# Kernel tuning notes

Hardware: AMD Instinct MI355X
Metric: run time of the kernel (lower is better)

## Reference

```python
import jax, jax.numpy as jnp
import numpy as np

N, E, B = 20000, 320000, 2
IN, HID, HEADS, OUT = 32, 64, 4, 8
N_MP = 2
SLOPE = 0.2  # GATConv default negative_slope


def setup_inputs() -> dict:
    key = jax.random.key(0)
    ks = jax.random.split(key, 10)
    s = 0.1
    return {
        "h": jax.random.normal(ks[0], (B, N, IN), jnp.float32),
        "edge_index": jax.random.randint(ks[1], (2, E), 0, N),
        "W_enc": jax.random.normal(ks[2], (IN, HID), jnp.float32) * s,
        "b_enc": jnp.zeros((HID,), jnp.float32),
        "W_gat": jax.random.normal(ks[3], (HID, HEADS * HID), jnp.float32) * s,
        "a_l": jax.random.normal(ks[4], (HEADS, HID), jnp.float32) * s,
        "a_r": jax.random.normal(ks[5], (HEADS, HID), jnp.float32) * s,
        "b_gat": jnp.zeros((HEADS * HID,), jnp.float32),
        "W_res": jax.random.normal(ks[6], (HID, HID), jnp.float32) * s,
        "b_res": jnp.zeros((HID,), jnp.float32),
        "W_dec": jax.random.normal(ks[7], (HID, OUT), jnp.float32) * s,
        "b_dec": jnp.zeros((OUT,), jnp.float32),
    }


def _gat(x, src, dst, W_gat, a_l, a_r, b_gat):
    # x: [N, B, HID] -> per-head projected features [N, B, HEADS, HID]
    ft = (x @ W_gat).reshape(N, B, HEADS, HID)
    el = jnp.einsum("nbhd,hd->nbh", ft, a_l)  # src attention term
    er = jnp.einsum("nbhd,hd->nbh", ft, a_r)  # dst attention term
    e = el[src] + er[dst]                      # [E, B, HEADS]
    e = jnp.where(e > 0, e, SLOPE * e)         # LeakyReLU
    # segment softmax over incoming edges of each dst node
    m = jax.ops.segment_max(e, dst, num_segments=N)
    e = jnp.exp(e - m[dst])
    z = jax.ops.segment_sum(e, dst, num_segments=N)
    alpha = e / z[dst]                         # [E, B, HEADS]
    msg = alpha[..., None] * ft[src]           # [E, B, HEADS, HID]
    agg = jax.ops.segment_sum(msg, dst, num_segments=N)
    return agg + b_gat.reshape(HEADS, HID)     # [N, B, HEADS, HID]


def reference(h, edge_index, W_enc, b_enc, W_gat, a_l, a_r, b_gat,
              W_res, b_res, W_dec, b_dec):
    src, dst = edge_index[0], edge_index[1]
    x = jnp.transpose(h, (1, 0, 2))            # [N, B, IN]
    x = x @ W_enc + b_enc                      # encoder (dropout in eval = identity)
    for _ in range(N_MP):
        gat_out = _gat(x, src, dst, W_gat, a_l, a_r, b_gat)
        x = jax.nn.elu(gat_out.mean(-2) + x @ W_res + b_res)
    x = x @ W_dec + b_dec
    return jnp.transpose(x, (1, 0, 2))         # [B, N, OUT]
```

## Files before the change

kernel.cpp:

```cpp
#include <hip/hip_runtime.h>
#include <hip/hip_bf16.h>

#define N_NODES 20000
#define N_EDGES 320000
#define BATCH 2
#define IN_DIM 32
#define HID 64
#define HEADS 4
#define OUT_DIM 8
#define ROWS (N_NODES * BATCH)
#define SLOPE 0.2f

typedef __hip_bfloat16 bf16;
typedef short v8s __attribute__((ext_vector_type(8)));
typedef float v4f __attribute__((ext_vector_type(4)));

#define WS_XA       0
#define WS_XB       1280000
#define WS_ELA      2560000
#define WS_ERA      2720000
#define WS_ELB      2880000
#define WS_ERB      3040000
#define WS_DEG      3200000
#define WS_ROWSTART 3220032
#define WS_CUR      3240064
#define WS_CSRC     3260096
#define WS_WGBPK    3580096
#define WS_WRESBPK  3588288
#define WS_WX8PK    3590336
#define WS_WENCBPK  3590848
#define WS_WDECBPK  3591872
#define WS_BGM      3592384
#define WS_END      3592448

__device__ __forceinline__ float us2f(unsigned short u) {
    union { unsigned int i; float f; } z; z.i = ((unsigned int)u) << 16; return z.f;
}
__device__ __forceinline__ unsigned short f2us(float f) {
    bf16 b = __float2bfloat16(f);
    return *(unsigned short*)&b;
}
__device__ __forceinline__ float ld(const void* p, int i, int isbf) {
    if (isbf) return us2f(((const unsigned short*)p)[i]);
    return ((const float*)p)[i];
}
__device__ __forceinline__ float lrexp(float v) {
    v = v > 0.f ? v : SLOPE * v;
    return __expf(fminf(v, 60.f));
}

__device__ __forceinline__ int sniff64(const void* h) {
    const unsigned short* u = (const unsigned short*)h;
    int lane = threadIdx.x & 63;
    unsigned short v = u[2 * lane];
    int ef = (v >> 7) & 0xFF;
    unsigned long long m = __ballot(ef >= 100 && ef <= 150);
    return __popcll(m) >= 48;
}

__global__ __launch_bounds__(256) void k_prep(const void* __restrict__ h,
                                              const void* __restrict__ Wg,
                                              const void* __restrict__ al,
                                              const void* __restrict__ ar,
                                              const void* __restrict__ Wr,
                                              const void* __restrict__ We,
                                              const void* __restrict__ Wd,
                                              const void* __restrict__ bg,
                                              unsigned short* __restrict__ WgBpk,
                                              unsigned short* __restrict__ WresBpk,
                                              unsigned short* __restrict__ Wx8pk,
                                              unsigned short* __restrict__ WencBpk,
                                              unsigned short* __restrict__ WdecBpk,
                                              float* __restrict__ bgm,
                                              int* __restrict__ deg) {
    int t = threadIdx.x, b = blockIdx.x;
    if (b >= 18) {
        int base = (b - 18) * 1024 + t * 4;
#pragma unroll
        for (int i = 0; i < 4; i++)
            if (base + i < 20032) deg[base + i] = 0;
        return;
    }
    const int isbf = sniff64(h);
    if (b < 16) {
#pragma unroll
        for (int q = 0; q < 4; q++) {
            int idx = b * 1024 + q * 256 + t;
            int j = idx & 7, m16 = (idx >> 3) & 15, quad = (idx >> 7) & 3;
            int ks = (idx >> 9) & 1, ct = (idx >> 10) & 3, hh = (idx >> 12) & 3;
            int k = ks * 32 + quad * 8 + j;
            int c = hh * 64 + ct * 16 + m16;
            WgBpk[idx] = f2us(ld(Wg, k * 256 + c, isbf));
        }
    } else if (b == 16) {
#pragma unroll
        for (int q = 0; q < 4; q++) {
            int idx = q * 256 + t;
            int j = idx & 7, m16 = (idx >> 3) & 15, quad = (idx >> 7) & 3;
            int ks = (idx >> 9) & 1;
            int k = ks * 32 + quad * 8 + j;
            float v = 0.f;
            if (m16 < 8) {
                int hh = m16 & 3, lr = m16 >> 2;
                const void* a = lr ? ar : al;
                for (int d = 0; d < 64; d++)
                    v += ld(Wg, k * 256 + hh * 64 + d, isbf) * ld(a, hh * 64 + d, isbf);
            }
            Wx8pk[idx] = f2us(v);
        }
#pragma unroll
        for (int q = 0; q < 8; q++) {
            int idx = q * 256 + t;
            int j = idx & 7, m16 = (idx >> 3) & 15, quad = (idx >> 7) & 3, ct = idx >> 9;
            int k = quad * 8 + j;
            WencBpk[idx] = f2us(ld(We, k * 64 + ct * 16 + m16, isbf));
        }
#pragma unroll
        for (int q = 0; q < 4; q++) {
            int idx = q * 256 + t;
            int j = idx & 7, m16 = (idx >> 3) & 15, quad = (idx >> 7) & 3;
            int ks = (idx >> 9) & 1;
            int k = ks * 32 + quad * 8 + j;
            WdecBpk[idx] = (m16 < 8) ? f2us(ld(Wd, k * 8 + m16, isbf)) : (unsigned short)0;
        }
        if (t < 64) {
            float s = 0.f;
            for (int hh = 0; hh < 4; hh++) s += ld(bg, hh * 64 + t, isbf);
            bgm[t] = 0.25f * s;
        }
    } else {
#pragma unroll
        for (int q = 0; q < 16; q++) {
            int idx = q * 256 + t;
            int j = idx & 7, m16 = (idx >> 3) & 15, quad = (idx >> 7) & 3;
            int ks = (idx >> 9) & 1;
            int k = ks * 32 + quad * 8 + j;
            WresBpk[idx] = f2us(ld(Wr, k * 64 + ((idx >> 10) & 3) * 16 + m16, isbf));
        }
    }
}

__global__ __launch_bounds__(256) void k_hist(const int* __restrict__ dst, int* __restrict__ deg) {
    int e = blockIdx.x * 256 + threadIdx.x;
    if (e < N_EDGES) atomicAdd(&deg[dst[e]], 1);
}

__global__ __launch_bounds__(1024) void k_scan(const int* __restrict__ deg,
                                               int* __restrict__ rowstart,
                                               int* __restrict__ cursor) {
    __shared__ int ssum[1024];
    int t = threadIdx.x;
    int base = t * 20;
    int local[20];
    int s = 0;
#pragma unroll
    for (int i = 0; i < 20; i++) {
        int v = (base + i < N_NODES) ? deg[base + i] : 0;
        local[i] = s;
        s += v;
    }
    ssum[t] = s;
    __syncthreads();
    for (int off = 1; off < 1024; off <<= 1) {
        int v = (t >= off) ? ssum[t - off] : 0;
        __syncthreads();
        if (t >= off) ssum[t] += v;
        __syncthreads();
    }
    int prev = (t == 0) ? 0 : ssum[t - 1];
#pragma unroll
    for (int i = 0; i < 20; i++) {
        if (base + i < N_NODES) {
            int v = prev + local[i];
            rowstart[base + i] = v;
            cursor[base + i] = v;
        }
    }
    if (t == 1023) rowstart[N_NODES] = ssum[1023];
}

__global__ __launch_bounds__(256) void k_scatter(const int* __restrict__ src,
                                                 const int* __restrict__ dst,
                                                 int* __restrict__ cursor,
                                                 int* __restrict__ csrc) {
    int e = blockIdx.x * 256 + threadIdx.x;
    if (e >= N_EDGES) return;
    int pos = atomicAdd(&cursor[dst[e]], 1);
    csrc[pos] = src[e];
}

__global__ __launch_bounds__(256) void k_enc2(const void* __restrict__ h,
                                              const unsigned short* __restrict__ WencBpk,
                                              const void* __restrict__ benc,
                                              const unsigned short* __restrict__ Wx8pk,
                                              unsigned int* __restrict__ xb32,
                                              float* __restrict__ el,
                                              float* __restrict__ er) {
    const int isbf = sniff64(h);
    __shared__ unsigned short sXb[64 * 64];
    int t = threadIdx.x;
    int w = t >> 6, lane = t & 63, quad = lane >> 4, m16 = lane & 15;
    int row0 = blockIdx.x * 64;
    int grow = row0 + w * 16 + m16;
    int n = grow >> 1, b = grow & 1;

    v8s Af;
    size_t hb = (size_t)(b * N_NODES + n) * IN_DIM + quad * 8;
    if (isbf) {
        Af = *(const v8s*)((const unsigned short*)h + hb);
    } else {
        const float4* hp = (const float4*)((const float*)h + hb);
        float4 xa = hp[0], xbv = hp[1];
        Af[0] = (short)f2us(xa.x);  Af[1] = (short)f2us(xa.y);
        Af[2] = (short)f2us(xa.z);  Af[3] = (short)f2us(xa.w);
        Af[4] = (short)f2us(xbv.x); Af[5] = (short)f2us(xbv.y);
        Af[6] = (short)f2us(xbv.z); Af[7] = (short)f2us(xbv.w);
    }

    v4f acc[4];
#pragma unroll
    for (int ct = 0; ct < 4; ct++) {
        v8s Bf = *(const v8s*)(WencBpk + ((ct << 9) | (quad << 7) | (m16 << 3)));
        acc[ct] = __builtin_amdgcn_mfma_f32_16x16x32_bf16(Af, Bf, (v4f)(0.f), 0, 0, 0);
    }

#pragma unroll
    for (int ct = 0; ct < 4; ct++) {
        int col = ct * 16 + m16;
        float bv = ld(benc, col, isbf);
        float vr[4];
        int rloc0 = w * 16 + quad * 4;
#pragma unroll
        for (int r = 0; r < 4; r++) {
            vr[r] = acc[ct][r] + bv;
            sXb[(rloc0 + r) * 64 + col] = f2us(vr[r]);
        }
        int nd0 = (row0 + rloc0) >> 1;
        xb32[(size_t)nd0 * 64 + col] =
            (unsigned int)f2us(vr[0]) | ((unsigned int)f2us(vr[1]) << 16);
        xb32[(size_t)(nd0 + 1) * 64 + col] =
            (unsigned int)f2us(vr[2]) | ((unsigned int)f2us(vr[3]) << 16);
    }
    __syncthreads();
    v4f e8 = (v4f)(0.f);
#pragma unroll
    for (int ks = 0; ks < 2; ks++) {
        v8s Af2 = *(const v8s*)(sXb + (w * 16 + m16) * 64 + ks * 32 + quad * 8);
        v8s Bf = *(const v8s*)(Wx8pk + (((ks * 4 + quad) << 7) + (m16 << 3)));
        e8 = __builtin_amdgcn_mfma_f32_16x16x32_bf16(Af2, Bf, e8, 0, 0, 0);
    }
    if (m16 < 8) {
#pragma unroll
        for (int r = 0; r < 4; r++) {
            int gr = row0 + w * 16 + quad * 4 + r;
            float v = e8[r];
            if (m16 < 4) el[gr * 4 + m16] = v;
            else         er[gr * 4 + (m16 - 4)] = v;
        }
    }
}

__global__ __launch_bounds__(256) void k_round(const int* __restrict__ rowstart,
                                               const int* __restrict__ csrc,
                                               const float* __restrict__ el_in,
                                               const float* __restrict__ er_in,
                                               const unsigned int* __restrict__ x_in,
                                               const unsigned short* __restrict__ WgBpk,
                                               const unsigned short* __restrict__ WresBpk,
                                               const unsigned short* __restrict__ Wx8pk,
                                               const unsigned short* __restrict__ WdecBpk,
                                               const void* __restrict__ h,
                                               const void* __restrict__ br,
                                               const void* __restrict__ bd,
                                               const float* __restrict__ bgm,
                                               unsigned int* __restrict__ x_out,
                                               float* __restrict__ el_out,
                                               float* __restrict__ er_out,
                                               void* __restrict__ out,
                                               int emit) {
    const int isbf = sniff64(h);
    __shared__ unsigned short sAgg[4 * 16 * 64];
    __shared__ unsigned short sXb[16 * 64];
    int t = threadIdx.x;
    int w = t >> 6, lane = t & 63, quad = lane >> 4, m16 = lane & 15;
    int i8 = m16 & 15 & 7;

    int nA = blockIdx.x * 8 + w * 2;
    int begA = rowstart[nA], endA = rowstart[nA + 1], endB = rowstart[nA + 2];
    int begB = endA;
    int rowNode = (m16 < 8) ? nA : (nA + 1);
    float erv = er_in[rowNode * 8 + i8];
    int beg = (quad < 2) ? begA : begB;
    int end = (quad < 2) ? endA : endB;
    int off = ((quad & 1) << 3);
    int active = ((m16 < 8) == (quad < 2));
    int itA = (endA - begA + 15) >> 4;
    int itB = (endB - begB + 15) >> 4;
    int itmax = itA > itB ? itA : itB;

    v4f accB0[4], accB1[4], accW;
#pragma unroll
    for (int tl = 0; tl < 4; tl++) { accB0[tl] = (v4f)(0.f); accB1[tl] = (v4f)(0.f); }
    accW = (v4f)(0.f);
    v8s Bones;
#pragma unroll
    for (int j = 0; j < 8; j++) Bones[j] = (short)0x3F80;

    for (int it = 0; it < itmax; ++it) {
        int p0 = beg + it * 16 + off;
        int s[8];
#pragma unroll
        for (int j = 0; j < 8; j++) {
            int idx = p0 + j;
            s[j] = csrc[idx < end ? idx : 0];
        }
        v8s Af;
#pragma unroll
        for (int j = 0; j < 8; j++) {
            float wv = 0.f;
            if (active && (p0 + j < end))
                wv = lrexp(el_in[s[j] * 8 + i8] + erv);
            Af[j] = (short)f2us(wv);
        }
        accW = __builtin_amdgcn_mfma_f32_16x16x32_bf16(Af, Bones, accW, 0, 0, 0);
#pragma unroll
        for (int tl = 0; tl < 4; tl++) {
            v8s B0, B1;
#pragma unroll
            for (int j = 0; j < 8; j++) {
                unsigned int q = x_in[(size_t)s[j] * 64 + tl * 16 + m16];
                B0[j] = (short)(q & 0xffffu);
                B1[j] = (short)(q >> 16);
            }
            accB0[tl] = __builtin_amdgcn_mfma_f32_16x16x32_bf16(Af, B0, accB0[tl], 0, 0, 0);
            accB1[tl] = __builtin_amdgcn_mfma_f32_16x16x32_bf16(Af, B1, accB1[tl], 0, 0, 0);
        }
    }

    {
        int row16 = w * 4 + quad;
        int swz = (row16 & 7) << 3;
#pragma unroll
        for (int tl = 0; tl < 4; tl++) {
#pragma unroll
            for (int r = 0; r < 4; r++) {
                float wss = accW[r];
                float mine = (quad & 1) ? accB1[tl][r] : accB0[tl][r];
                float v = (wss > 0.f) ? mine / (4.f * wss) : 0.f;
                int col = tl * 16 + m16;
                sAgg[((r * 16 + row16) << 6) | (col ^ swz)] = f2us(v);
            }
        }
    }
    __syncthreads();

    int grow0 = blockIdx.x * 16;
    int grow = grow0 + m16;
    int nd = grow >> 1;
    unsigned sh = (grow & 1) * 16;
    int ct = w;

    v4f acc = (v4f)(0.f);
#pragma unroll
    for (int hh = 0; hh < 4; hh++) {
#pragma unroll
        for (int ks = 0; ks < 2; ks++) {
            int si = ((hh * 16 + m16) << 6) | ((ks * 32 + quad * 8) ^ ((m16 & 7) << 3));
            v8s Af = *(const v8s*)(sAgg + si);
            v8s Bf = *(const v8s*)(WgBpk + ((hh << 12) | (ct << 10) | (ks << 9) | (quad << 7) | (m16 << 3)));
            acc = __builtin_amdgcn_mfma_f32_16x16x32_bf16(Af, Bf, acc, 0, 0, 0);
        }
    }
#pragma unroll
    for (int ks = 0; ks < 2; ks++) {
        const uint4* xp = (const uint4*)(x_in + (size_t)nd * 64 + ks * 32 + quad * 8);
        uint4 qa = xp[0], qb = xp[1];
        v8s Af;
        Af[0] = (short)((qa.x >> sh) & 0xffffu);
        Af[1] = (short)((qa.y >> sh) & 0xffffu);
        Af[2] = (short)((qa.z >> sh) & 0xffffu);
        Af[3] = (short)((qa.w >> sh) & 0xffffu);
        Af[4] = (short)((qb.x >> sh) & 0xffffu);
        Af[5] = (short)((qb.y >> sh) & 0xffffu);
        Af[6] = (short)((qb.z >> sh) & 0xffffu);
        Af[7] = (short)((qb.w >> sh) & 0xffffu);
        v8s Bf = *(const v8s*)(WresBpk + ((ct << 10) | (ks << 9) | (quad << 7) | (m16 << 3)));
        acc = __builtin_amdgcn_mfma_f32_16x16x32_bf16(Af, Bf, acc, 0, 0, 0);
    }

    {
        int col = ct * 16 + m16;
        float bv = ld(br, col, isbf) + bgm[col];
        float vr[4];
#pragma unroll
        for (int r = 0; r < 4; r++) {
            float v = acc[r] + bv;
            v = v > 0.f ? v : expm1f(v);
            vr[r] = v;
            sXb[(quad * 4 + r) * 64 + col] = f2us(v);
        }
        if (emit) {
            int nd0 = (grow0 + quad * 4) >> 1;
            x_out[(size_t)nd0 * 64 + col] =
                (unsigned int)f2us(vr[0]) | ((unsigned int)f2us(vr[1]) << 16);
            x_out[(size_t)(nd0 + 1) * 64 + col] =
                (unsigned int)f2us(vr[2]) | ((unsigned int)f2us(vr[3]) << 16);
        }
    }
    __syncthreads();

    if (w == 0) {
        if (emit) {
            v4f e8 = (v4f)(0.f);
#pragma unroll
            for (int ks = 0; ks < 2; ks++) {
                v8s Af = *(const v8s*)(sXb + m16 * 64 + ks * 32 + quad * 8);
                v8s Bf = *(const v8s*)(Wx8pk + (((ks * 4 + quad) << 7) + (m16 << 3)));
                e8 = __builtin_amdgcn_mfma_f32_16x16x32_bf16(Af, Bf, e8, 0, 0, 0);
            }
            if (m16 < 8) {
#pragma unroll
                for (int r = 0; r < 4; r++) {
                    int gr = grow0 + quad * 4 + r;
                    float v = e8[r];
                    if (m16 < 4) el_out[gr * 4 + m16] = v;
                    else         er_out[gr * 4 + (m16 - 4)] = v;
                }
            }
        } else {
            v4f o8 = (v4f)(0.f);
#pragma unroll
            for (int ks = 0; ks < 2; ks++) {
                v8s Af = *(const v8s*)(sXb + m16 * 64 + ks * 32 + quad * 8);
                v8s Bf = *(const v8s*)(WdecBpk + ((ks << 9) | (quad << 7) | (m16 << 3)));
                o8 = __builtin_amdgcn_mfma_f32_16x16x32_bf16(Af, Bf, o8, 0, 0, 0);
            }
            if (m16 < 8) {
                float bvd = ld(bd, m16, isbf);
#pragma unroll
                for (int r = 0; r < 4; r++) {
                    int gr = grow0 + quad * 4 + r;
                    int nn = gr >> 1, bb = gr & 1;
                    size_t oi = (size_t)(bb * N_NODES + nn) * OUT_DIM + m16;
                    float v = o8[r] + bvd;
                    if (isbf) ((unsigned short*)out)[oi] = f2us(v);
                    else      ((float*)out)[oi] = v;
                }
            }
        }
    }
}

extern "C" void kernel_launch(void* const* d_in, const int* in_sizes, int n_in,
                              void* d_out, int out_size, void* d_ws, size_t ws_size,
                              hipStream_t stream) {
    const void* h     = d_in[0];
    const int*  ei    = (const int*)d_in[1];
    const void* W_enc = d_in[2];
    const void* b_enc = d_in[3];
    const void* W_gat = d_in[4];
    const void* a_l   = d_in[5];
    const void* a_r   = d_in[6];
    const void* b_gat = d_in[7];
    const void* W_res = d_in[8];
    const void* b_res = d_in[9];
    const void* W_dec = d_in[10];
    const void* b_dec = d_in[11];

    float* ws = (float*)d_ws;
    unsigned int* xA = (unsigned int*)(ws + WS_XA);
    unsigned int* xB = (unsigned int*)(ws + WS_XB);
    float* elA      = ws + WS_ELA;
    float* erA      = ws + WS_ERA;
    float* elB      = ws + WS_ELB;
    float* erB      = ws + WS_ERB;
    int*   deg      = (int*)(ws + WS_DEG);
    int*   rowstart = (int*)(ws + WS_ROWSTART);
    int*   cursor   = (int*)(ws + WS_CUR);
    int*   csrc     = (int*)(ws + WS_CSRC);
    unsigned short* WgBpk   = (unsigned short*)(ws + WS_WGBPK);
    unsigned short* WresBpk = (unsigned short*)(ws + WS_WRESBPK);
    unsigned short* Wx8pk   = (unsigned short*)(ws + WS_WX8PK);
    unsigned short* WencBpk = (unsigned short*)(ws + WS_WENCBPK);
    unsigned short* WdecBpk = (unsigned short*)(ws + WS_WDECBPK);
    float* bgm      = ws + WS_BGM;

    const int* src = ei;
    const int* dst = ei + N_EDGES;

    k_prep<<<38, 256, 0, stream>>>(h, W_gat, a_l, a_r, W_res, W_enc, W_dec, b_gat,
                                   WgBpk, WresBpk, Wx8pk, WencBpk, WdecBpk, bgm, deg);
    k_hist<<<(N_EDGES + 255) / 256, 256, 0, stream>>>(dst, deg);
    k_scan<<<1, 1024, 0, stream>>>(deg, rowstart, cursor);
    k_scatter<<<(N_EDGES + 255) / 256, 256, 0, stream>>>(src, dst, cursor, csrc);

    k_enc2<<<ROWS / 64, 256, 0, stream>>>(h, WencBpk, b_enc, Wx8pk, xA, elA, erA);

    k_round<<<N_NODES / 8, 256, 0, stream>>>(rowstart, csrc, elA, erA, xA,
                                             WgBpk, WresBpk, Wx8pk, WdecBpk,
                                             h, b_res, b_dec, bgm,
                                             xB, elB, erB, d_out, 1);
    k_round<<<N_NODES / 8, 256, 0, stream>>>(rowstart, csrc, elB, erB, xB,
                                             WgBpk, WresBpk, Wx8pk, WdecBpk,
                                             h, b_res, b_dec, bgm,
                                             xA, elA, erA, d_out, 0);
}
```

Before: 238.6 us.

## Fuse all stages into one persistent cooperative kernel with grid syncs

```diff
diff --git a/kernel.cpp b/kernel.cpp
--- a/kernel.cpp
+++ b/kernel.cpp
@@ -1,5 +1,8 @@
 #include <hip/hip_runtime.h>
 #include <hip/hip_bf16.h>
+#include <hip/hip_cooperative_groups.h>
+
+namespace cg = cooperative_groups;
 
 #define N_NODES 20000
 #define N_EDGES 320000
@@ -10,6 +13,9 @@
 #define OUT_DIM 8
 #define ROWS (N_NODES * BATCH)
 #define SLOPE 0.2f
+
+#define GRID 768
+#define TPB 256
 
 typedef __hip_bfloat16 bf16;
 typedef short v8s __attribute__((ext_vector_type(8)));
@@ -31,7 +37,8 @@
 #define WS_WENCBPK  3590848
 #define WS_WDECBPK  3591872
 #define WS_BGM      3592384
-#define WS_END      3592448
+#define WS_PART     3592448
+#define WS_END      3593216
 
 __device__ __forceinline__ float us2f(unsigned short u) {
     union { unsigned int i; float f; } z; z.i = ((unsigned int)u) << 16; return z.f;
@@ -57,6 +64,460 @@
     unsigned long long m = __ballot(ef >= 100 && ef <= 150);
     return __popcll(m) >= 48;
 }
+
+
+__device__ __forceinline__ void prep_body(int b, int isbf,
+                                          const void* __restrict__ Wg,
+                                          const void* __restrict__ al,
+                                          const void* __restrict__ ar,
+                                          const void* __restrict__ Wr,
+                                          const void* __restrict__ We,
+                                          const void* __restrict__ Wd,
+                                          const void* __restrict__ bg,
+                                          unsigned short* __restrict__ WgBpk,
+                                          unsigned short* __restrict__ WresBpk,
+                                          unsigned short* __restrict__ Wx8pk,
+                                          unsigned short* __restrict__ WencBpk,
+                                          unsigned short* __restrict__ WdecBpk,
+                                          float* __restrict__ bgm,
+                                          int* __restrict__ deg) {
+    int t = threadIdx.x;
+    if (b >= 18) {
+        int base = (b - 18) * 1024 + t * 4;
+#pragma unroll
+        for (int i = 0; i < 4; i++)
+            if (base + i < 20032) deg[base + i] = 0;
+        return;
+    }
+    if (b < 16) {
+#pragma unroll
+        for (int q = 0; q < 4; q++) {
+            int idx = b * 1024 + q * 256 + t;
+            int j = idx & 7, m16 = (idx >> 3) & 15, quad = (idx >> 7) & 3;
+            int ks = (idx >> 9) & 1, ct = (idx >> 10) & 3, hh = (idx >> 12) & 3;
+            int k = ks * 32 + quad * 8 + j;
+            int c = hh * 64 + ct * 16 + m16;
+            WgBpk[idx] = f2us(ld(Wg, k * 256 + c, isbf));
+        }
+    } else if (b == 16) {
+#pragma unroll
+        for (int q = 0; q < 4; q++) {
+            int idx = q * 256 + t;
+            int j = idx & 7, m16 = (idx >> 3) & 15, quad = (idx >> 7) & 3;
+            int ks = (idx >> 9) & 1;
+            int k = ks * 32 + quad * 8 + j;
+            float v = 0.f;
+            if (m16 < 8) {
+                int hh = m16 & 3, lr = m16 >> 2;
+                const void* a = lr ? ar : al;
+                for (int d = 0; d < 64; d++)
+                    v += ld(Wg, k * 256 + hh * 64 + d, isbf) * ld(a, hh * 64 + d, isbf);
+            }
+            Wx8pk[idx] = f2us(v);
+        }
+#pragma unroll
+        for (int q = 0; q < 8; q++) {
+            int idx = q * 256 + t;
+            int j = idx & 7, m16 = (idx >> 3) & 15, quad = (idx >> 7) & 3, ct = idx >> 9;
+            int k = quad * 8 + j;
+            WencBpk[idx] = f2us(ld(We, k * 64 + ct * 16 + m16, isbf));
+        }
+#pragma unroll
+        for (int q = 0; q < 4; q++) {
+            int idx = q * 256 + t;
+            int j = idx & 7, m16 = (idx >> 3) & 15, quad = (idx >> 7) & 3;
+            int ks = (idx >> 9) & 1;
+            int k = ks * 32 + quad * 8 + j;
+            WdecBpk[idx] = (m16 < 8) ? f2us(ld(Wd, k * 8 + m16, isbf)) : (unsigned short)0;
+        }
+        if (t < 64) {
+            float s = 0.f;
+            for (int hh = 0; hh < 4; hh++) s += ld(bg, hh * 64 + t, isbf);
+            bgm[t] = 0.25f * s;
+        }
+    } else {
+#pragma unroll
+        for (int q = 0; q < 16; q++) {
+            int idx = q * 256 + t;
+            int j = idx & 7, m16 = (idx >> 3) & 15, quad = (idx >> 7) & 3;
+            int ks = (idx >> 9) & 1;
+            int k = ks * 32 + quad * 8 + j;
+            WresBpk[idx] = f2us(ld(Wr, k * 64 + ((idx >> 10) & 3) * 16 + m16, isbf));
+        }
+    }
+}
+
+__device__ __forceinline__ void enc_unit(int u, int isbf,
+                                         const void* __restrict__ h,
+                                         const unsigned short* __restrict__ WencBpk,
+                                         const void* __restrict__ benc,
+                                         const unsigned short* __restrict__ Wx8pk,
+                                         unsigned int* __restrict__ xb32,
+                                         float* __restrict__ el,
+                                         float* __restrict__ er,
+                                         unsigned short* __restrict__ sXb) {
+    int t = threadIdx.x;
+    int w = t >> 6, lane = t & 63, quad = lane >> 4, m16 = lane & 15;
+    int row0 = u * 64;
+    int grow = row0 + w * 16 + m16;
+    int n = grow >> 1, b = grow & 1;
+
+    v8s Af;
+    size_t hb = (size_t)(b * N_NODES + n) * IN_DIM + quad * 8;
+    if (isbf) {
+        Af = *(const v8s*)((const unsigned short*)h + hb);
+    } else {
+        const float4* hp = (const float4*)((const float*)h + hb);
+        float4 xa = hp[0], xbv = hp[1];
+        Af[0] = (short)f2us(xa.x);  Af[1] = (short)f2us(xa.y);
+        Af[2] = (short)f2us(xa.z);  Af[3] = (short)f2us(xa.w);
+        Af[4] = (short)f2us(xbv.x); Af[5] = (short)f2us(xbv.y);
+        Af[6] = (short)f2us(xbv.z); Af[7] = (short)f2us(xbv.w);
+    }
+
+    v4f acc[4];
+#pragma unroll
+    for (int ct = 0; ct < 4; ct++) {
+        v8s Bf = *(const v8s*)(WencBpk + ((ct << 9) | (quad << 7) | (m16 << 3)));
+        acc[ct] = __builtin_amdgcn_mfma_f32_16x16x32_bf16(Af, Bf, (v4f)(0.f), 0, 0, 0);
+    }
+
+#pragma unroll
+    for (int ct = 0; ct < 4; ct++) {
+        int col = ct * 16 + m16;
+        float bv = ld(benc, col, isbf);
+        float vr[4];
+        int rloc0 = w * 16 + quad * 4;
+#pragma unroll
+        for (int r = 0; r < 4; r++) {
+            vr[r] = acc[ct][r] + bv;
+            sXb[(rloc0 + r) * 64 + col] = f2us(vr[r]);
+        }
+        int nd0 = (row0 + rloc0) >> 1;
+        xb32[(size_t)nd0 * 64 + col] =
+            (unsigned int)f2us(vr[0]) | ((unsigned int)f2us(vr[1]) << 16);
+        xb32[(size_t)(nd0 + 1) * 64 + col] =
+            (unsigned int)f2us(vr[2]) | ((unsigned int)f2us(vr[3]) << 16);
+    }
+    __syncthreads();
+    v4f e8 = (v4f)(0.f);
+#pragma unroll
+    for (int ks = 0; ks < 2; ks++) {
+        v8s Af2 = *(const v8s*)(sXb + (w * 16 + m16) * 64 + ks * 32 + quad * 8);
+        v8s Bf = *(const v8s*)(Wx8pk + (((ks * 4 + quad) << 7) + (m16 << 3)));
+        e8 = __builtin_amdgcn_mfma_f32_16x16x32_bf16(Af2, Bf, e8, 0, 0, 0);
+    }
+    if (m16 < 8) {
+#pragma unroll
+        for (int r = 0; r < 4; r++) {
+            int gr = row0 + w * 16 + quad * 4 + r;
+            float v = e8[r];
+            if (m16 < 4) el[gr * 4 + m16] = v;
+            else         er[gr * 4 + (m16 - 4)] = v;
+        }
+    }
+}
+
+__device__ __forceinline__ void round_unit(int u, int isbf,
+                                           const int* __restrict__ rowstart,
+                                           const int* __restrict__ csrc,
+                                           const float* __restrict__ el_in,
+                                           const float* __restrict__ er_in,
+                                           const unsigned int* __restrict__ x_in,
+                                           const unsigned short* __restrict__ WgBpk,
+                                           const unsigned short* __restrict__ WresBpk,
+                                           const unsigned short* __restrict__ Wx8pk,
+                                           const unsigned short* __restrict__ WdecBpk,
+                                           const void* __restrict__ br,
+                                           const void* __restrict__ bd,
+                                           const float* __restrict__ bgm,
+                                           unsigned int* __restrict__ x_out,
+                                           float* __restrict__ el_out,
+                                           float* __restrict__ er_out,
+                                           void* __restrict__ out,
+                                           int emit,
+                                           unsigned short* __restrict__ sAgg,
+                                           unsigned short* __restrict__ sXb) {
+    int t = threadIdx.x;
+    int w = t >> 6, lane = t & 63, quad = lane >> 4, m16 = lane & 15;
+    int i8 = m16 & 7;
+
+    int nA = u * 8 + w * 2;
+    int begA = rowstart[nA], endA = rowstart[nA + 1], endB = rowstart[nA + 2];
+    int begB = endA;
+    int rowNode = (m16 < 8) ? nA : (nA + 1);
+    float erv = er_in[rowNode * 8 + i8];
+    int beg = (quad < 2) ? begA : begB;
+    int end = (quad < 2) ? endA : endB;
+    int off = ((quad & 1) << 3);
+    int active = ((m16 < 8) == (quad < 2));
+    int itA = (endA - begA + 15) >> 4;
+    int itB = (endB - begB + 15) >> 4;
+    int itmax = itA > itB ? itA : itB;
+
+    v4f accB0[4], accB1[4], accW;
+#pragma unroll
+    for (int tl = 0; tl < 4; tl++) { accB0[tl] = (v4f)(0.f); accB1[tl] = (v4f)(0.f); }
+    accW = (v4f)(0.f);
+    v8s Bones;
+#pragma unroll
+    for (int j = 0; j < 8; j++) Bones[j] = (short)0x3F80;
+
+    for (int it = 0; it < itmax; ++it) {
+        int p0 = beg + it * 16 + off;
+        int s[8];
+#pragma unroll
+        for (int j = 0; j < 8; j++) {
+            int idx = p0 + j;
+            s[j] = csrc[idx < end ? idx : 0];
+        }
+        v8s Af;
+#pragma unroll
+        for (int j = 0; j < 8; j++) {
+            float wv = 0.f;
+            if (active && (p0 + j < end))
+                wv = lrexp(el_in[s[j] * 8 + i8] + erv);
+            Af[j] = (short)f2us(wv);
+        }
+        accW = __builtin_amdgcn_mfma_f32_16x16x32_bf16(Af, Bones, accW, 0, 0, 0);
+#pragma unroll
+        for (int tl = 0; tl < 4; tl++) {
+            v8s B0, B1;
+#pragma unroll
+            for (int j = 0; j < 8; j++) {
+                unsigned int q = x_in[(size_t)s[j] * 64 + tl * 16 + m16];
+                B0[j] = (short)(q & 0xffffu);
+                B1[j] = (short)(q >> 16);
+            }
+            accB0[tl] = __builtin_amdgcn_mfma_f32_16x16x32_bf16(Af, B0, accB0[tl], 0, 0, 0);
+            accB1[tl] = __builtin_amdgcn_mfma_f32_16x16x32_bf16(Af, B1, accB1[tl], 0, 0, 0);
+        }
+    }
+
+    {
+        int row16 = w * 4 + quad;
+        int swz = (row16 & 7) << 3;
+#pragma unroll
+        for (int tl = 0; tl < 4; tl++) {
+#pragma unroll
+            for (int r = 0; r < 4; r++) {
+                float wss = accW[r];
+                float mine = (quad & 1) ? accB1[tl][r] : accB0[tl][r];
+                float v = (wss > 0.f) ? mine / (4.f * wss) : 0.f;
+                int col = tl * 16 + m16;
+                sAgg[((r * 16 + row16) << 6) | (col ^ swz)] = f2us(v);
+            }
+        }
+    }
+    __syncthreads();
+
+    int grow0 = u * 16;
+    int grow = grow0 + m16;
+    int nd = grow >> 1;
+    unsigned sh = (grow & 1) * 16;
+    int ct = w;
+
+    v4f acc = (v4f)(0.f);
+#pragma unroll
+    for (int hh = 0; hh < 4; hh++) {
+#pragma unroll
+        for (int ks = 0; ks < 2; ks++) {
+            int si = ((hh * 16 + m16) << 6) | ((ks * 32 + quad * 8) ^ ((m16 & 7) << 3));
+            v8s Af = *(const v8s*)(sAgg + si);
+            v8s Bf = *(const v8s*)(WgBpk + ((hh << 12) | (ct << 10) | (ks << 9) | (quad << 7) | (m16 << 3)));
+            acc = __builtin_amdgcn_mfma_f32_16x16x32_bf16(Af, Bf, acc, 0, 0, 0);
+        }
+    }
+#pragma unroll
+    for (int ks = 0; ks < 2; ks++) {
+        const uint4* xp = (const uint4*)(x_in + (size_t)nd * 64 + ks * 32 + quad * 8);
+        uint4 qa = xp[0], qb = xp[1];
+        v8s Af;
+        Af[0] = (short)((qa.x >> sh) & 0xffffu);
+        Af[1] = (short)((qa.y >> sh) & 0xffffu);
+        Af[2] = (short)((qa.z >> sh) & 0xffffu);
+        Af[3] = (short)((qa.w >> sh) & 0xffffu);
+        Af[4] = (short)((qb.x >> sh) & 0xffffu);
+        Af[5] = (short)((qb.y >> sh) & 0xffffu);
+        Af[6] = (short)((qb.z >> sh) & 0xffffu);
+        Af[7] = (short)((qb.w >> sh) & 0xffffu);
+        v8s Bf = *(const v8s*)(WresBpk + ((ct << 10) | (ks << 9) | (quad << 7) | (m16 << 3)));
+        acc = __builtin_amdgcn_mfma_f32_16x16x32_bf16(Af, Bf, acc, 0, 0, 0);
+    }
+
+    {
+        int col = ct * 16 + m16;
+        float bv = ld(br, col, isbf) + bgm[col];
+        float vr[4];
+#pragma unroll
+        for (int r = 0; r < 4; r++) {
+            float v = acc[r] + bv;
+            v = v > 0.f ? v : expm1f(v);
+            vr[r] = v;
+            sXb[(quad * 4 + r) * 64 + col] = f2us(v);
+        }
+        if (emit) {
+            int nd0 = (grow0 + quad * 4) >> 1;
+            x_out[(size_t)nd0 * 64 + col] =
+                (unsigned int)f2us(vr[0]) | ((unsigned int)f2us(vr[1]) << 16);
+            x_out[(size_t)(nd0 + 1) * 64 + col] =
+                (unsigned int)f2us(vr[2]) | ((unsigned int)f2us(vr[3]) << 16);
+        }
+    }
+    __syncthreads();
+
+    if (w == 0) {
+        if (emit) {
+            v4f e8 = (v4f)(0.f);
+#pragma unroll
+            for (int ks = 0; ks < 2; ks++) {
+                v8s Af = *(const v8s*)(sXb + m16 * 64 + ks * 32 + quad * 8);
+                v8s Bf = *(const v8s*)(Wx8pk + (((ks * 4 + quad) << 7) + (m16 << 3)));
+                e8 = __builtin_amdgcn_mfma_f32_16x16x32_bf16(Af, Bf, e8, 0, 0, 0);
+            }
+            if (m16 < 8) {
+#pragma unroll
+                for (int r = 0; r < 4; r++) {
+                    int gr = grow0 + quad * 4 + r;
+                    float v = e8[r];
+                    if (m16 < 4) el_out[gr * 4 + m16] = v;
+                    else         er_out[gr * 4 + (m16 - 4)] = v;
+                }
+            }
+        } else {
+            v4f o8 = (v4f)(0.f);
+#pragma unroll
+            for (int ks = 0; ks < 2; ks++) {
+                v8s Af = *(const v8s*)(sXb + m16 * 64 + ks * 32 + quad * 8);
+                v8s Bf = *(const v8s*)(WdecBpk + ((ks << 9) | (quad << 7) | (m16 << 3)));
+                o8 = __builtin_amdgcn_mfma_f32_16x16x32_bf16(Af, Bf, o8, 0, 0, 0);
+            }
+            if (m16 < 8) {
+                float bvd = ld(bd, m16, isbf);
+#pragma unroll
+                for (int r = 0; r < 4; r++) {
+                    int gr = grow0 + quad * 4 + r;
+                    int nn = gr >> 1, bb = gr & 1;
+                    size_t oi = (size_t)(bb * N_NODES + nn) * OUT_DIM + m16;
+                    float v = o8[r] + bvd;
+                    if (isbf) ((unsigned short*)out)[oi] = f2us(v);
+                    else      ((float*)out)[oi] = v;
+                }
+            }
+        }
+    }
+}
+
+__global__ __launch_bounds__(TPB, 3) void k_all(const void* __restrict__ h,
+                                                const int* __restrict__ ei,
+                                                const void* __restrict__ W_enc,
+                                                const void* __restrict__ b_enc,
+                                                const void* __restrict__ W_gat,
+                                                const void* __restrict__ a_l,
+                                                const void* __restrict__ a_r,
+                                                const void* __restrict__ b_gat,
+                                                const void* __restrict__ W_res,
+                                                const void* __restrict__ b_res,
+                                                const void* __restrict__ W_dec,
+                                                const void* __restrict__ b_dec,
+                                                float* __restrict__ ws,
+                                                void* __restrict__ out) {
+    cg::grid_group gg = cg::this_grid();
+    __shared__ unsigned short smem[5120];
+    unsigned short* sAgg = smem;
+    unsigned short* sXb  = smem + 4096;
+
+    unsigned int* xA = (unsigned int*)(ws + WS_XA);
+    unsigned int* xB = (unsigned int*)(ws + WS_XB);
+    float* elA      = ws + WS_ELA;
+    float* erA      = ws + WS_ERA;
+    float* elB      = ws + WS_ELB;
+    float* erB      = ws + WS_ERB;
+    int*   deg      = (int*)(ws + WS_DEG);
+    int*   rowstart = (int*)(ws + WS_ROWSTART);
+    int*   cursor   = (int*)(ws + WS_CUR);
+    int*   csrc     = (int*)(ws + WS_CSRC);
+    int*   part     = (int*)(ws + WS_PART);
+    unsigned short* WgBpk   = (unsigned short*)(ws + WS_WGBPK);
+    unsigned short* WresBpk = (unsigned short*)(ws + WS_WRESBPK);
+    unsigned short* Wx8pk   = (unsigned short*)(ws + WS_WX8PK);
+    unsigned short* WencBpk = (unsigned short*)(ws + WS_WENCBPK);
+    unsigned short* WdecBpk = (unsigned short*)(ws + WS_WDECBPK);
+    float* bgm      = ws + WS_BGM;
+
+    const int* srcp = ei;
+    const int* dstp = ei + N_EDGES;
+    const int isbf = sniff64(h);
+    const int t = threadIdx.x;
+    const int b = blockIdx.x;
+
+    if (b < 38)
+        prep_body(b, isbf, W_gat, a_l, a_r, W_res, W_enc, W_dec, b_gat,
+                  WgBpk, WresBpk, Wx8pk, WencBpk, WdecBpk, bgm, deg);
+    gg.sync();
+
+    for (int e = b * TPB + t; e < N_EDGES; e += GRID * TPB)
+        atomicAdd(&deg[dstp[e]], 1);
+    gg.sync();
+
+    if (t < 64) {
+        if (b < 500) {
+            int v = (t < 40) ? deg[b * 40 + t] : 0;
+            for (int d = 32; d; d >>= 1) v += __shfl_down(v, d);
+            if (t == 0) part[b] = v;
+        } else if (t == 0) {
+            part[b] = 0;
+        }
+    }
+    gg.sync();
+
+    if (b < 500 && t < 64) {
+        int o = 0;
+        for (int j = t; j < b; j += 64) o += part[j];
+        for (int d = 32; d; d >>= 1) o += __shfl_down(o, d);
+        o = __shfl(o, 0);
+        int i = b * 40 + t;
+        int v = (t < 40) ? deg[i] : 0;
+        int incl = v;
+        for (int d = 1; d < 64; d <<= 1) {
+            int uu = __shfl_up(incl, d);
+            if (t >= d) incl += uu;
+        }
+        if (t < 40) {
+            int rs = o + incl - v;
+            rowstart[i] = rs;
+            cursor[i] = rs;
+            if (b == 499 && t == 39) rowstart[N_NODES] = o + incl;
+        }
+    }
+    gg.sync();
+
+    for (int e = b * TPB + t; e < N_EDGES; e += GRID * TPB) {
+        int pos = atomicAdd(&cursor[dstp[e]], 1);
+        csrc[pos] = srcp[e];
+    }
+    for (int u = b; u < ROWS / 64; u += GRID) {
+        __syncthreads();
+        enc_unit(u, isbf, h, WencBpk, b_enc, Wx8pk, xA, elA, erA, smem);
+    }
+    gg.sync();
+
+    for (int u = b; u < N_NODES / 8; u += GRID) {
+        __syncthreads();
+        round_unit(u, isbf, rowstart, csrc, elA, erA, xA,
+                   WgBpk, WresBpk, Wx8pk, WdecBpk, b_res, b_dec, bgm,
+                   xB, elB, erB, out, 1, sAgg, sXb);
+    }
+    gg.sync();
+
+    for (int u = b; u < N_NODES / 8; u += GRID) {
+        __syncthreads();
+        round_unit(u, isbf, rowstart, csrc, elB, erB, xB,
+                   WgBpk, WresBpk, Wx8pk, WdecBpk, b_res, b_dec, bgm,
+                   xA, elA, erA, out, 0, sAgg, sXb);
+    }
+}
+
 
 __global__ __launch_bounds__(256) void k_prep(const void* __restrict__ h,
                                               const void* __restrict__ Wg,
@@ -73,71 +534,9 @@
                                               unsigned short* __restrict__ WdecBpk,
                                               float* __restrict__ bgm,
                                               int* __restrict__ deg) {
-    int t = threadIdx.x, b = blockIdx.x;
-    if (b >= 18) {
-        int base = (b - 18) * 1024 + t * 4;
-#pragma unroll
-        for (int i = 0; i < 4; i++)
-            if (base + i < 20032) deg[base + i] = 0;
-        return;
-    }
-    const int isbf = sniff64(h);
-    if (b < 16) {
-#pragma unroll
-        for (int q = 0; q < 4; q++) {
-            int idx = b * 1024 + q * 256 + t;
-            int j = idx & 7, m16 = (idx >> 3) & 15, quad = (idx >> 7) & 3;
-            int ks = (idx >> 9) & 1, ct = (idx >> 10) & 3, hh = (idx >> 12) & 3;
-            int k = ks * 32 + quad * 8 + j;
-            int c = hh * 64 + ct * 16 + m16;
-            WgBpk[idx] = f2us(ld(Wg, k * 256 + c, isbf));
-        }
-    } else if (b == 16) {
-#pragma unroll
-        for (int q = 0; q < 4; q++) {
-            int idx = q * 256 + t;
-            int j = idx & 7, m16 = (idx >> 3) & 15, quad = (idx >> 7) & 3;
-            int ks = (idx >> 9) & 1;
-            int k = ks * 32 + quad * 8 + j;
-            float v = 0.f;
-            if (m16 < 8) {
-                int hh = m16 & 3, lr = m16 >> 2;
-                const void* a = lr ? ar : al;
-                for (int d = 0; d < 64; d++)
-                    v += ld(Wg, k * 256 + hh * 64 + d, isbf) * ld(a, hh * 64 + d, isbf);
-            }
-            Wx8pk[idx] = f2us(v);
-        }
-#pragma unroll
-        for (int q = 0; q < 8; q++) {
-            int idx = q * 256 + t;
-            int j = idx & 7, m16 = (idx >> 3) & 15, quad = (idx >> 7) & 3, ct = idx >> 9;
-            int k = quad * 8 + j;
-            WencBpk[idx] = f2us(ld(We, k * 64 + ct * 16 + m16, isbf));
-        }
-#pragma unroll
-        for (int q = 0; q < 4; q++) {
-            int idx = q * 256 + t;
-            int j = idx & 7, m16 = (idx >> 3) & 15, quad = (idx >> 7) & 3;
-            int ks = (idx >> 9) & 1;
-            int k = ks * 32 + quad * 8 + j;
-            WdecBpk[idx] = (m16 < 8) ? f2us(ld(Wd, k * 8 + m16, isbf)) : (unsigned short)0;
-        }
-        if (t < 64) {
-            float s = 0.f;
-            for (int hh = 0; hh < 4; hh++) s += ld(bg, hh * 64 + t, isbf);
-            bgm[t] = 0.25f * s;
-        }
-    } else {
-#pragma unroll
-        for (int q = 0; q < 16; q++) {
-            int idx = q * 256 + t;
-            int j = idx & 7, m16 = (idx >> 3) & 15, quad = (idx >> 7) & 3;
-            int ks = (idx >> 9) & 1;
-            int k = ks * 32 + quad * 8 + j;
-            WresBpk[idx] = f2us(ld(Wr, k * 64 + ((idx >> 10) & 3) * 16 + m16, isbf));
-        }
-    }
+    const int isbf = (blockIdx.x < 18) ? sniff64(h) : 0;
+    prep_body(blockIdx.x, isbf, Wg, al, ar, Wr, We, Wd, bg,
+              WgBpk, WresBpk, Wx8pk, WencBpk, WdecBpk, bgm, deg);
 }
 
 __global__ __launch_bounds__(256) void k_hist(const int* __restrict__ dst, int* __restrict__ deg) {
@@ -198,66 +597,7 @@
                                               float* __restrict__ er) {
     const int isbf = sniff64(h);
     __shared__ unsigned short sXb[64 * 64];
-    int t = threadIdx.x;
-    int w = t >> 6, lane = t & 63, quad = lane >> 4, m16 = lane & 15;
-    int row0 = blockIdx.x * 64;
-    int grow = row0 + w * 16 + m16;
-    int n = grow >> 1, b = grow & 1;
-
-    v8s Af;
-    size_t hb = (size_t)(b * N_NODES + n) * IN_DIM + quad * 8;
-    if (isbf) {
-        Af = *(const v8s*)((const unsigned short*)h + hb);
-    } else {
-        const float4* hp = (const float4*)((const float*)h + hb);
-        float4 xa = hp[0], xbv = hp[1];
-        Af[0] = (short)f2us(xa.x);  Af[1] = (short)f2us(xa.y);
-        Af[2] = (short)f2us(xa.z);  Af[3] = (short)f2us(xa.w);
-        Af[4] = (short)f2us(xbv.x); Af[5] = (short)f2us(xbv.y);
-        Af[6] = (short)f2us(xbv.z); Af[7] = (short)f2us(xbv.w);
-    }
-
-    v4f acc[4];
-#pragma unroll
-    for (int ct = 0; ct < 4; ct++) {
-        v8s Bf = *(const v8s*)(WencBpk + ((ct << 9) | (quad << 7) | (m16 << 3)));
-        acc[ct] = __builtin_amdgcn_mfma_f32_16x16x32_bf16(Af, Bf, (v4f)(0.f), 0, 0, 0);
-    }
-
-#pragma unroll
-    for (int ct = 0; ct < 4; ct++) {
-        int col = ct * 16 + m16;
-        float bv = ld(benc, col, isbf);
-        float vr[4];
-        int rloc0 = w * 16 + quad * 4;
-#pragma unroll
-        for (int r = 0; r < 4; r++) {
-            vr[r] = acc[ct][r] + bv;
-            sXb[(rloc0 + r) * 64 + col] = f2us(vr[r]);
-        }
-        int nd0 = (row0 + rloc0) >> 1;
-        xb32[(size_t)nd0 * 64 + col] =
-            (unsigned int)f2us(vr[0]) | ((unsigned int)f2us(vr[1]) << 16);
-        xb32[(size_t)(nd0 + 1) * 64 + col] =
-            (unsigned int)f2us(vr[2]) | ((unsigned int)f2us(vr[3]) << 16);
-    }
-    __syncthreads();
-    v4f e8 = (v4f)(0.f);
-#pragma unroll
-    for (int ks = 0; ks < 2; ks++) {
-        v8s Af2 = *(const v8s*)(sXb + (w * 16 + m16) * 64 + ks * 32 + quad * 8);
-        v8s Bf = *(const v8s*)(Wx8pk + (((ks * 4 + quad) << 7) + (m16 << 3)));
-        e8 = __builtin_amdgcn_mfma_f32_16x16x32_bf16(Af2, Bf, e8, 0, 0, 0);
-    }
-    if (m16 < 8) {
-#pragma unroll
-        for (int r = 0; r < 4; r++) {
-            int gr = row0 + w * 16 + quad * 4 + r;
-            float v = e8[r];
-            if (m16 < 4) el[gr * 4 + m16] = v;
-            else         er[gr * 4 + (m16 - 4)] = v;
-        }
-    }
+    enc_unit(blockIdx.x, isbf, h, WencBpk, benc, Wx8pk, xb32, el, er, sXb);
 }
 
 __global__ __launch_bounds__(256) void k_round(const int* __restrict__ rowstart,
@@ -279,176 +619,10 @@
                                                void* __restrict__ out,
                                                int emit) {
     const int isbf = sniff64(h);
-    __shared__ unsigned short sAgg[4 * 16 * 64];
-    __shared__ unsigned short sXb[16 * 64];
-    int t = threadIdx.x;
-    int w = t >> 6, lane = t & 63, quad = lane >> 4, m16 = lane & 15;
-    int i8 = m16 & 15 & 7;
-
-    int nA = blockIdx.x * 8 + w * 2;
-    int begA = rowstart[nA], endA = rowstart[nA + 1], endB = rowstart[nA + 2];
-    int begB = endA;
-    int rowNode = (m16 < 8) ? nA : (nA + 1);
-    float erv = er_in[rowNode * 8 + i8];
-    int beg = (quad < 2) ? begA : begB;
-    int end = (quad < 2) ? endA : endB;
-    int off = ((quad & 1) << 3);
-    int active = ((m16 < 8) == (quad < 2));
-    int itA = (endA - begA + 15) >> 4;
-    int itB = (endB - begB + 15) >> 4;
-    int itmax = itA > itB ? itA : itB;
-
-    v4f accB0[4], accB1[4], accW;
-#pragma unroll
-    for (int tl = 0; tl < 4; tl++) { accB0[tl] = (v4f)(0.f); accB1[tl] = (v4f)(0.f); }
-    accW = (v4f)(0.f);
-    v8s Bones;
-#pragma unroll
-    for (int j = 0; j < 8; j++) Bones[j] = (short)0x3F80;
-
-    for (int it = 0; it < itmax; ++it) {
-        int p0 = beg + it * 16 + off;
-        int s[8];
-#pragma unroll
-        for (int j = 0; j < 8; j++) {
-            int idx = p0 + j;
-            s[j] = csrc[idx < end ? idx : 0];
-        }
-        v8s Af;
-#pragma unroll
-        for (int j = 0; j < 8; j++) {
-            float wv = 0.f;
-            if (active && (p0 + j < end))
-                wv = lrexp(el_in[s[j] * 8 + i8] + erv);
-            Af[j] = (short)f2us(wv);
-        }
-        accW = __builtin_amdgcn_mfma_f32_16x16x32_bf16(Af, Bones, accW, 0, 0, 0);
-#pragma unroll
-        for (int tl = 0; tl < 4; tl++) {
-            v8s B0, B1;
-#pragma unroll
-            for (int j = 0; j < 8; j++) {
-                unsigned int q = x_in[(size_t)s[j] * 64 + tl * 16 + m16];
-                B0[j] = (short)(q & 0xffffu);
-                B1[j] = (short)(q >> 16);
-            }
-            accB0[tl] = __builtin_amdgcn_mfma_f32_16x16x32_bf16(Af, B0, accB0[tl], 0, 0, 0);
-            accB1[tl] = __builtin_amdgcn_mfma_f32_16x16x32_bf16(Af, B1, accB1[tl], 0, 0, 0);
-        }
-    }
-
-    {
-        int row16 = w * 4 + quad;
-        int swz = (row16 & 7) << 3;
-#pragma unroll
-        for (int tl = 0; tl < 4; tl++) {
-#pragma unroll
-            for (int r = 0; r < 4; r++) {
-                float wss = accW[r];
-                float mine = (quad & 1) ? accB1[tl][r] : accB0[tl][r];
-                float v = (wss > 0.f) ? mine / (4.f * wss) : 0.f;
-                int col = tl * 16 + m16;
-                sAgg[((r * 16 + row16) << 6) | (col ^ swz)] = f2us(v);
-            }
-        }
-    }
-    __syncthreads();
-
-    int grow0 = blockIdx.x * 16;
-    int grow = grow0 + m16;
-    int nd = grow >> 1;
-    unsigned sh = (grow & 1) * 16;
-    int ct = w;
-
-    v4f acc = (v4f)(0.f);
-#pragma unroll
-    for (int hh = 0; hh < 4; hh++) {
-#pragma unroll
-        for (int ks = 0; ks < 2; ks++) {
-            int si = ((hh * 16 + m16) << 6) | ((ks * 32 + quad * 8) ^ ((m16 & 7) << 3));
-            v8s Af = *(const v8s*)(sAgg + si);
-            v8s Bf = *(const v8s*)(WgBpk + ((hh << 12) | (ct << 10) | (ks << 9) | (quad << 7) | (m16 << 3)));
-            acc = __builtin_amdgcn_mfma_f32_16x16x32_bf16(Af, Bf, acc, 0, 0, 0);
-        }
-    }
-#pragma unroll
-    for (int ks = 0; ks < 2; ks++) {
-        const uint4* xp = (const uint4*)(x_in + (size_t)nd * 64 + ks * 32 + quad * 8);
-        uint4 qa = xp[0], qb = xp[1];
-        v8s Af;
-        Af[0] = (short)((qa.x >> sh) & 0xffffu);
-        Af[1] = (short)((qa.y >> sh) & 0xffffu);
-        Af[2] = (short)((qa.z >> sh) & 0xffffu);
-        Af[3] = (short)((qa.w >> sh) & 0xffffu);
-        Af[4] = (short)((qb.x >> sh) & 0xffffu);
-        Af[5] = (short)((qb.y >> sh) & 0xffffu);
-        Af[6] = (short)((qb.z >> sh) & 0xffffu);
-        Af[7] = (short)((qb.w >> sh) & 0xffffu);
-        v8s Bf = *(const v8s*)(WresBpk + ((ct << 10) | (ks << 9) | (quad << 7) | (m16 << 3)));
-        acc = __builtin_amdgcn_mfma_f32_16x16x32_bf16(Af, Bf, acc, 0, 0, 0);
-    }
-
-    {
-        int col = ct * 16 + m16;
-        float bv = ld(br, col, isbf) + bgm[col];
-        float vr[4];
-#pragma unroll
-        for (int r = 0; r < 4; r++) {
-            float v = acc[r] + bv;
-            v = v > 0.f ? v : expm1f(v);
-            vr[r] = v;
-            sXb[(quad * 4 + r) * 64 + col] = f2us(v);
-        }
-        if (emit) {
-            int nd0 = (grow0 + quad * 4) >> 1;
-            x_out[(size_t)nd0 * 64 + col] =
-                (unsigned int)f2us(vr[0]) | ((unsigned int)f2us(vr[1]) << 16);
-            x_out[(size_t)(nd0 + 1) * 64 + col] =
-                (unsigned int)f2us(vr[2]) | ((unsigned int)f2us(vr[3]) << 16);
-        }
-    }
-    __syncthreads();
-
-    if (w == 0) {
-        if (emit) {
-            v4f e8 = (v4f)(0.f);
-#pragma unroll
-            for (int ks = 0; ks < 2; ks++) {
-                v8s Af = *(const v8s*)(sXb + m16 * 64 + ks * 32 + quad * 8);
-                v8s Bf = *(const v8s*)(Wx8pk + (((ks * 4 + quad) << 7) + (m16 << 3)));
-                e8 = __builtin_amdgcn_mfma_f32_16x16x32_bf16(Af, Bf, e8, 0, 0, 0);
-            }
-            if (m16 < 8) {
-#pragma unroll
-                for (int r = 0; r < 4; r++) {
-                    int gr = grow0 + quad * 4 + r;
-                    float v = e8[r];
-                    if (m16 < 4) el_out[gr * 4 + m16] = v;
-                    else         er_out[gr * 4 + (m16 - 4)] = v;
-                }
-            }
-        } else {
-            v4f o8 = (v4f)(0.f);
-#pragma unroll
-            for (int ks = 0; ks < 2; ks++) {
-                v8s Af = *(const v8s*)(sXb + m16 * 64 + ks * 32 + quad * 8);
-                v8s Bf = *(const v8s*)(WdecBpk + ((ks << 9) | (quad << 7) | (m16 << 3)));
-                o8 = __builtin_amdgcn_mfma_f32_16x16x32_bf16(Af, Bf, o8, 0, 0, 0);
-            }
-            if (m16 < 8) {
-                float bvd = ld(bd, m16, isbf);
-#pragma unroll
-                for (int r = 0; r < 4; r++) {
-                    int gr = grow0 + quad * 4 + r;
-                    int nn = gr >> 1, bb = gr & 1;
-                    size_t oi = (size_t)(bb * N_NODES + nn) * OUT_DIM + m16;
-                    float v = o8[r] + bvd;
-                    if (isbf) ((unsigned short*)out)[oi] = f2us(v);
-                    else      ((float*)out)[oi] = v;
-                }
-            }
-        }
-    }
+    __shared__ unsigned short smem[5120];
+    round_unit(blockIdx.x, isbf, rowstart, csrc, el_in, er_in, x_in,
+               WgBpk, WresBpk, Wx8pk, WdecBpk, br, bd, bgm,
+               x_out, el_out, er_out, out, emit, smem, smem + 4096);
 }
 
 extern "C" void kernel_launch(void* const* d_in, const int* in_sizes, int n_in,
@@ -468,6 +642,17 @@
     const void* b_dec = d_in[11];
 
     float* ws = (float*)d_ws;
+    void* outp = d_out;
+
+    void* kargs[] = { (void*)&h, (void*)&ei, (void*)&W_enc, (void*)&b_enc,
+                      (void*)&W_gat, (void*)&a_l, (void*)&a_r, (void*)&b_gat,
+                      (void*)&W_res, (void*)&b_res, (void*)&W_dec, (void*)&b_dec,
+                      (void*)&ws, (void*)&outp };
+    hipError_t err = hipLaunchCooperativeKernel(k_all, dim3(GRID), dim3(TPB),
+                                                kargs, 0, stream);
+    if (err == hipSuccess) return;
+    (void)hipGetLastError();
+
     unsigned int* xA = (unsigned int*)(ws + WS_XA);
     unsigned int* xB = (unsigned int*)(ws + WS_XB);
     float* elA      = ws + WS_ELA;
@@ -493,9 +678,7 @@
     k_hist<<<(N_EDGES + 255) / 256, 256, 0, stream>>>(dst, deg);
     k_scan<<<1, 1024, 0, stream>>>(deg, rowstart, cursor);
     k_scatter<<<(N_EDGES + 255) / 256, 256, 0, stream>>>(src, dst, cursor, csrc);
-
     k_enc2<<<ROWS / 64, 256, 0, stream>>>(h, WencBpk, b_enc, Wx8pk, xA, elA, erA);
-
     k_round<<<N_NODES / 8, 256, 0, stream>>>(rowstart, csrc, elA, erA, xA,
                                              WgBpk, WresBpk, Wx8pk, WdecBpk,
                                              h, b_res, b_dec, bgm,
```

After: 742.8 us. +211.3%, slower.
